# Kernel optimization log

Hardware: AMD Instinct MI355X
Metric: run time of the kernel (lower is better)

The kernel has to match this reference:

```python
import jax, jax.numpy as jnp
import numpy as np

N_NODES = 50000
N_EDGES = 800000
D_IN = 64
D_OUT = 64
EPS = 0.0  # DGL GINConv default init_eps=0, not learnable


def setup_inputs() -> dict:
    key = jax.random.key(0)
    k1, k2, k3, k4, k5 = jax.random.split(key, 5)
    node_inputs = jax.random.normal(k1, (N_NODES, D_IN), dtype=jnp.float32)
    src = jax.random.randint(k2, (N_EDGES,), 0, N_NODES, dtype=jnp.int64)
    dst = jax.random.randint(k3, (N_EDGES,), 0, N_NODES, dtype=jnp.int64)
    # nn.Linear(in_feats, out_feats) params (PyTorch layout: W [out, in])
    bound = 1.0 / np.sqrt(D_IN)
    W = jax.random.uniform(k4, (D_OUT, D_IN), dtype=jnp.float32, minval=-bound, maxval=bound)
    b = jax.random.uniform(k5, (D_OUT,), dtype=jnp.float32, minval=-bound, maxval=bound)
    return {"node_inputs": node_inputs, "W": W, "b": b, "src": src, "dst": dst}


def reference(node_inputs, W, b, src, dst):
    # GIN sum aggregation: for each node, sum features of in-neighbors
    # messages: [E, D_IN] gathered, scatter-summed into [N, D_IN]
    agg = jax.ops.segment_sum(node_inputs[src], dst, num_segments=N_NODES)
    h = (1.0 + EPS) * node_inputs + agg          # [N, D_IN]
    h = h @ W.T + b                              # Linear -> [N, D_OUT]
    h = jnp.tanh(h)
    # Dropout is identity in eval mode (deterministic reference)
    return h
```

## Files before the change

### kernel.cpp

```cpp
#include <hip/hip_runtime.h>
#include <hip/hip_fp16.h>

#define N_NODES 50000
#define N_EDGES 800000
#define D 64

#define NBIN 512
#define BINW 98
#define PBLK 160
#define EPB  5000
#define CAPB 26
#define NCAP 64
#define WGROUP 260

typedef int iv4 __attribute__((ext_vector_type(4)));

__global__ __launch_bounds__(512) void gin_part(const float* __restrict__ x,
                                                const int* __restrict__ src,
                                                const int* __restrict__ dst,
                                                unsigned int* __restrict__ regions,
                                                int* __restrict__ bincnt,
                                                __half* __restrict__ xh) {
    __shared__ int lcnt[NBIN];
    const int tid = threadIdx.x;
    if (tid < NBIN) lcnt[tid] = 0;
    __syncthreads();

    const int ebase = blockIdx.x * EPB;
    unsigned int* __restrict__ rbase = regions + (size_t)blockIdx.x * NBIN * CAPB;

    for (int i = tid; i < EPB / 4; i += 512) {
        const int e = ebase + i * 4;
        const iv4 d4 = *(const iv4*)&dst[e];
        const iv4 s4 = *(const iv4*)&src[e];
        const int dd[4] = {d4.x, d4.y, d4.z, d4.w};
        const int ss[4] = {s4.x, s4.y, s4.z, s4.w};
        #pragma unroll
        for (int j = 0; j < 4; ++j) {
            const int bin = dd[j] / BINW;
            const int pos = atomicAdd(&lcnt[bin], 1);
            if (pos < CAPB)
                rbase[bin * CAPB + pos] = ((unsigned)dd[j] << 16) | (unsigned)ss[j];
        }
    }
    __syncthreads();
    if (tid < NBIN) bincnt[blockIdx.x * NBIN + tid] = lcnt[tid] < CAPB ? lcnt[tid] : CAPB;

    union Pk { uint2 u; __half2 h[2]; };
    uint2* __restrict__ xo = (uint2*)xh;
    for (int i = blockIdx.x * 512 + tid; i < (N_NODES * D) / 4; i += PBLK * 512) {
        const float4 v = *(const float4*)&x[(size_t)i * 4];
        Pk p;
        p.h[0] = __floats2half2_rn(v.x, v.y);
        p.h[1] = __floats2half2_rn(v.z, v.w);
        xo[i] = p.u;
    }
}

__device__ __forceinline__ float fast_tanh(float v) {
    return 1.0f - 2.0f / (__expf(2.0f * v) + 1.0f);
}

__global__ __launch_bounds__(1024, 8) void gin_node(const float* __restrict__ x,
                                                 const __half* __restrict__ xh,
                                                 const float* __restrict__ W,
                                                 const float* __restrict__ bias,
                                                 const unsigned int* __restrict__ regions,
                                                 const int* __restrict__ bincnt,
                                                 float* __restrict__ out) {
    __shared__ alignas(16) unsigned short sbuck[BINW * NCAP];
    __shared__ int   lcnt[BINW];
    __shared__ float Wt2[16 * WGROUP];
    __shared__ float hs[16][4][68];

    const int tid  = threadIdx.x;
    const int lane = tid & 63;
    const int wv   = tid >> 6;
    const int sub  = lane >> 4;
    const int q    = lane & 15;
    const int b    = blockIdx.x;
    const int lo   = b * BINW;

    if (tid < BINW) lcnt[tid] = 0;
    #pragma unroll
    for (int i = tid; i < D * D; i += 1024) {
        const int f = i >> 6, k = i & 63;
        Wt2[(k >> 2) * WGROUP + (f << 2) + (k & 3)] = W[i];
    }
    __syncthreads();

    const int g2 = lane >> 5;
    const int l2 = lane & 31;
    for (int p2 = wv; p2 < PBLK / 2; p2 += 16) {
        const int pb = p2 * 2 + g2;
        const int n = bincnt[pb * NBIN + b];
        if (l2 < n) {
            const unsigned e = regions[((size_t)pb * NBIN + b) * CAPB + l2];
            const int dl  = (int)(e >> 16) - lo;
            const int pos = atomicAdd(&lcnt[dl], 1);
            if (pos < NCAP) sbuck[dl * NCAP + pos] = (unsigned short)(e & 0xffffu);
        }
    }
    __syncthreads();

    const uint2* __restrict__ xr = (const uint2*)xh;
    const float bf = bias[lane];
    const int ncnt   = (wv < 2) ? 7 : 6;
    const int nstart = wv * 6 + ((wv < 2) ? wv : 2);
    const int nend   = nstart + ncnt;

    union Pk { uint2 u; __half2 h[2]; };

    for (int base = nstart; base < nend; base += 4) {
        const int li    = base + sub;
        const bool nv   = (li < nend);
        const int  liC  = nv ? li : (nend - 1);
        const int  node = lo + liC;
        const bool ndv  = nv && (node < N_NODES);
        const int  nodeC = (node < N_NODES) ? node : (N_NODES - 1);

        float4 acc = *(const float4*)&x[(size_t)nodeC * D + (q << 2)];

        int cn = ndv ? lcnt[liC] : 0;
        if (cn > NCAP) cn = NCAP;
        const uint4* __restrict__ slv = (const uint4*)&sbuck[liC * NCAP];

        for (int i = 0; i < cn; i += 8) {
            const int rem = cn - i;
            const uint4 iw = slv[i >> 3];
            int s0 = (int)(iw.x & 0xffffu), s1 = (int)(iw.x >> 16);
            int s2 = (int)(iw.y & 0xffffu), s3 = (int)(iw.y >> 16);
            int s4 = (int)(iw.z & 0xffffu), s5 = (int)(iw.z >> 16);
            int s6 = (int)(iw.w & 0xffffu), s7 = (int)(iw.w >> 16);
            s1 = (1 < rem) ? s1 : 0;  s2 = (2 < rem) ? s2 : 0;
            s3 = (3 < rem) ? s3 : 0;  s4 = (4 < rem) ? s4 : 0;
            s5 = (5 < rem) ? s5 : 0;  s6 = (6 < rem) ? s6 : 0;
            s7 = (7 < rem) ? s7 : 0;
            Pk u0, u1, u2, u3, u4, u5, u6, u7;
            u0.u = xr[(size_t)s0 * 16 + q];  u1.u = xr[(size_t)s1 * 16 + q];
            u2.u = xr[(size_t)s2 * 16 + q];  u3.u = xr[(size_t)s3 * 16 + q];
            u4.u = xr[(size_t)s4 * 16 + q];  u5.u = xr[(size_t)s5 * 16 + q];
            u6.u = xr[(size_t)s6 * 16 + q];  u7.u = xr[(size_t)s7 * 16 + q];
            const float m1 = (1 < rem) ? 1.f : 0.f;
            const float m2 = (2 < rem) ? 1.f : 0.f;
            const float m3 = (3 < rem) ? 1.f : 0.f;
            const float m4 = (4 < rem) ? 1.f : 0.f;
            const float m5 = (5 < rem) ? 1.f : 0.f;
            const float m6 = (6 < rem) ? 1.f : 0.f;
            const float m7 = (7 < rem) ? 1.f : 0.f;
            {
                const float2 a = __half22float2(u0.h[0]), c = __half22float2(u0.h[1]);
                acc.x += a.x; acc.y += a.y; acc.z += c.x; acc.w += c.y;
            }
            {
                const float2 a = __half22float2(u1.h[0]), c = __half22float2(u1.h[1]);
                acc.x = fmaf(a.x, m1, acc.x); acc.y = fmaf(a.y, m1, acc.y);
                acc.z = fmaf(c.x, m1, acc.z); acc.w = fmaf(c.y, m1, acc.w);
            }
            {
                const float2 a = __half22float2(u2.h[0]), c = __half22float2(u2.h[1]);
                acc.x = fmaf(a.x, m2, acc.x); acc.y = fmaf(a.y, m2, acc.y);
                acc.z = fmaf(c.x, m2, acc.z); acc.w = fmaf(c.y, m2, acc.w);
            }
            {
                const float2 a = __half22float2(u3.h[0]), c = __half22float2(u3.h[1]);
                acc.x = fmaf(a.x, m3, acc.x); acc.y = fmaf(a.y, m3, acc.y);
                acc.z = fmaf(c.x, m3, acc.z); acc.w = fmaf(c.y, m3, acc.w);
            }
            {
                const float2 a = __half22float2(u4.h[0]), c = __half22float2(u4.h[1]);
                acc.x = fmaf(a.x, m4, acc.x); acc.y = fmaf(a.y, m4, acc.y);
                acc.z = fmaf(c.x, m4, acc.z); acc.w = fmaf(c.y, m4, acc.w);
            }
            {
                const float2 a = __half22float2(u5.h[0]), c = __half22float2(u5.h[1]);
                acc.x = fmaf(a.x, m5, acc.x); acc.y = fmaf(a.y, m5, acc.y);
                acc.z = fmaf(c.x, m5, acc.z); acc.w = fmaf(c.y, m5, acc.w);
            }
            {
                const float2 a = __half22float2(u6.h[0]), c = __half22float2(u6.h[1]);
                acc.x = fmaf(a.x, m6, acc.x); acc.y = fmaf(a.y, m6, acc.y);
                acc.z = fmaf(c.x, m6, acc.z); acc.w = fmaf(c.y, m6, acc.w);
            }
            {
                const float2 a = __half22float2(u7.h[0]), c = __half22float2(u7.h[1]);
                acc.x = fmaf(a.x, m7, acc.x); acc.y = fmaf(a.y, m7, acc.y);
                acc.z = fmaf(c.x, m7, acc.z); acc.w = fmaf(c.y, m7, acc.w);
            }
        }
        *(float4*)&hs[wv][sub][q << 2] = acc;

        const int left = nend - base;
        const int mcnt = left < 4 ? left : 4;
        const int n0 = lo + base;
        {
            float4 rA = {bf, 0.f, 0.f, 0.f}, rB = rA;
            #pragma unroll 4
            for (int kg = 0; kg < 16; ++kg) {
                const float4 w  = *(const float4*)&Wt2[kg * WGROUP + (lane << 2)];
                const float4 hA = *(const float4*)&hs[wv][0][kg << 2];
                const float4 hB = *(const float4*)&hs[wv][1][kg << 2];
                rA.x = fmaf(hA.x, w.x, rA.x); rA.y = fmaf(hA.y, w.y, rA.y);
                rA.z = fmaf(hA.z, w.z, rA.z); rA.w = fmaf(hA.w, w.w, rA.w);
                rB.x = fmaf(hB.x, w.x, rB.x); rB.y = fmaf(hB.y, w.y, rB.y);
                rB.z = fmaf(hB.z, w.z, rB.z); rB.w = fmaf(hB.w, w.w, rB.w);
            }
            if (n0 < N_NODES)
                out[(size_t)n0 * D + lane] = fast_tanh((rA.x + rA.y) + (rA.z + rA.w));
            if (1 < mcnt && n0 + 1 < N_NODES)
                out[(size_t)(n0 + 1) * D + lane] = fast_tanh((rB.x + rB.y) + (rB.z + rB.w));
        }
        if (2 < mcnt) {
            float4 rC = {bf, 0.f, 0.f, 0.f}, rD = rC;
            #pragma unroll 4
            for (int kg = 0; kg < 16; ++kg) {
                const float4 w  = *(const float4*)&Wt2[kg * WGROUP + (lane << 2)];
                const float4 hC = *(const float4*)&hs[wv][2][kg << 2];
                const float4 hD = *(const float4*)&hs[wv][3][kg << 2];
                rC.x = fmaf(hC.x, w.x, rC.x); rC.y = fmaf(hC.y, w.y, rC.y);
                rC.z = fmaf(hC.z, w.z, rC.z); rC.w = fmaf(hC.w, w.w, rC.w);
                rD.x = fmaf(hD.x, w.x, rD.x); rD.y = fmaf(hD.y, w.y, rD.y);
                rD.z = fmaf(hD.z, w.z, rD.z); rD.w = fmaf(hD.w, w.w, rD.w);
            }
            if (n0 + 2 < N_NODES)
                out[(size_t)(n0 + 2) * D + lane] = fast_tanh((rC.x + rC.y) + (rC.z + rC.w));
            if (3 < mcnt && n0 + 3 < N_NODES)
                out[(size_t)(n0 + 3) * D + lane] = fast_tanh((rD.x + rD.y) + (rD.z + rD.w));
        }
    }
}

extern "C" void kernel_launch(void* const* d_in, const int* in_sizes, int n_in,
                              void* d_out, int out_size, void* d_ws, size_t ws_size,
                              hipStream_t stream) {
    const float* x    = (const float*)d_in[0];
    const float* W    = (const float*)d_in[1];
    const float* bias = (const float*)d_in[2];
    const int*   src  = (const int*)d_in[3];
    const int*   dst  = (const int*)d_in[4];
    float*       out  = (float*)d_out;

    unsigned int* regions = (unsigned int*)d_ws;
    int*          bincnt  = (int*)(regions + (size_t)PBLK * NBIN * CAPB);
    __half*       xh      = (__half*)(bincnt + PBLK * NBIN);

    gin_part<<<PBLK, 512, 0, stream>>>(x, src, dst, regions, bincnt, xh);
    gin_node<<<NBIN, 1024, 0, stream>>>(x, xh, W, bias, regions, bincnt, out);
}
```

Measured before the change: 109.4 us.

## Gather all wave nodes in one pass with 8 lanes per node and 16-byte loads

Each wavefront now gathers neighbor features for all 6-7 of its nodes at once, using 8 lanes per node and 16-byte fp16 loads, instead of two passes of 4 nodes with 16 lanes each. The transform stage is unrolled into fixed pairs of node rows plus an optional seventh. This aims to remove the second gather pass and its serialized latency, and to cut the number of load instructions. In exchange each lane holds more accumulators and the inner loop is only 4 deep, giving fewer loads in flight per iteration and higher register pressure.

After: 112.0 us. 1.02x slower.

```diff
diff --git a/kernel.cpp b/kernel.cpp
--- a/kernel.cpp
+++ b/kernel.cpp
@@ -71,13 +71,13 @@
     __shared__ alignas(16) unsigned short sbuck[BINW * NCAP];
     __shared__ int   lcnt[BINW];
     __shared__ float Wt2[16 * WGROUP];
-    __shared__ float hs[16][4][68];
+    __shared__ float hs[16][8][68];
 
     const int tid  = threadIdx.x;
     const int lane = tid & 63;
     const int wv   = tid >> 6;
-    const int sub  = lane >> 4;
-    const int q    = lane & 15;
+    const int sub8 = lane >> 3;
+    const int q8   = lane & 7;
     const int b    = blockIdx.x;
     const int lo   = b * BINW;
 
@@ -103,130 +103,140 @@
     }
     __syncthreads();
 
-    const uint2* __restrict__ xr = (const uint2*)xh;
+    const uint4* __restrict__ xq = (const uint4*)xh;
     const float bf = bias[lane];
     const int ncnt   = (wv < 2) ? 7 : 6;
     const int nstart = wv * 6 + ((wv < 2) ? wv : 2);
     const int nend   = nstart + ncnt;
 
-    union Pk { uint2 u; __half2 h[2]; };
-
-    for (int base = nstart; base < nend; base += 4) {
-        const int li    = base + sub;
+    union Pk4 { uint4 u; __half2 h[4]; };
+
+    {
+        const int li    = nstart + sub8;
         const bool nv   = (li < nend);
         const int  liC  = nv ? li : (nend - 1);
         const int  node = lo + liC;
         const bool ndv  = nv && (node < N_NODES);
         const int  nodeC = (node < N_NODES) ? node : (N_NODES - 1);
 
-        float4 acc = *(const float4*)&x[(size_t)nodeC * D + (q << 2)];
+        float4 accA = *(const float4*)&x[(size_t)nodeC * D + (q8 << 3)];
+        float4 accB = *(const float4*)&x[(size_t)nodeC * D + (q8 << 3) + 4];
 
         int cn = ndv ? lcnt[liC] : 0;
         if (cn > NCAP) cn = NCAP;
-        const uint4* __restrict__ slv = (const uint4*)&sbuck[liC * NCAP];
-
-        for (int i = 0; i < cn; i += 8) {
+        const uint2* __restrict__ sl2 = (const uint2*)&sbuck[liC * NCAP];
+
+        for (int i = 0; i < cn; i += 4) {
             const int rem = cn - i;
-            const uint4 iw = slv[i >> 3];
+            const uint2 iw = sl2[i >> 2];
             int s0 = (int)(iw.x & 0xffffu), s1 = (int)(iw.x >> 16);
             int s2 = (int)(iw.y & 0xffffu), s3 = (int)(iw.y >> 16);
-            int s4 = (int)(iw.z & 0xffffu), s5 = (int)(iw.z >> 16);
-            int s6 = (int)(iw.w & 0xffffu), s7 = (int)(iw.w >> 16);
             s1 = (1 < rem) ? s1 : 0;  s2 = (2 < rem) ? s2 : 0;
-            s3 = (3 < rem) ? s3 : 0;  s4 = (4 < rem) ? s4 : 0;
-            s5 = (5 < rem) ? s5 : 0;  s6 = (6 < rem) ? s6 : 0;
-            s7 = (7 < rem) ? s7 : 0;
-            Pk u0, u1, u2, u3, u4, u5, u6, u7;
-            u0.u = xr[(size_t)s0 * 16 + q];  u1.u = xr[(size_t)s1 * 16 + q];
-            u2.u = xr[(size_t)s2 * 16 + q];  u3.u = xr[(size_t)s3 * 16 + q];
-            u4.u = xr[(size_t)s4 * 16 + q];  u5.u = xr[(size_t)s5 * 16 + q];
-            u6.u = xr[(size_t)s6 * 16 + q];  u7.u = xr[(size_t)s7 * 16 + q];
+            s3 = (3 < rem) ? s3 : 0;
+            Pk4 u0, u1, u2, u3;
+            u0.u = xq[(size_t)s0 * 8 + q8];  u1.u = xq[(size_t)s1 * 8 + q8];
+            u2.u = xq[(size_t)s2 * 8 + q8];  u3.u = xq[(size_t)s3 * 8 + q8];
             const float m1 = (1 < rem) ? 1.f : 0.f;
             const float m2 = (2 < rem) ? 1.f : 0.f;
             const float m3 = (3 < rem) ? 1.f : 0.f;
-            const float m4 = (4 < rem) ? 1.f : 0.f;
-            const float m5 = (5 < rem) ? 1.f : 0.f;
-            const float m6 = (6 < rem) ? 1.f : 0.f;
-            const float m7 = (7 < rem) ? 1.f : 0.f;
             {
                 const float2 a = __half22float2(u0.h[0]), c = __half22float2(u0.h[1]);
-                acc.x += a.x; acc.y += a.y; acc.z += c.x; acc.w += c.y;
+                const float2 e = __half22float2(u0.h[2]), g = __half22float2(u0.h[3]);
+                accA.x += a.x; accA.y += a.y; accA.z += c.x; accA.w += c.y;
+                accB.x += e.x; accB.y += e.y; accB.z += g.x; accB.w += g.y;
             }
             {
                 const float2 a = __half22float2(u1.h[0]), c = __half22float2(u1.h[1]);
-                acc.x = fmaf(a.x, m1, acc.x); acc.y = fmaf(a.y, m1, acc.y);
-                acc.z = fmaf(c.x, m1, acc.z); acc.w = fmaf(c.y, m1, acc.w);
+                const float2 e = __half22float2(u1.h[2]), g = __half22float2(u1.h[3]);
+                accA.x = fmaf(a.x, m1, accA.x); accA.y = fmaf(a.y, m1, accA.y);
+                accA.z = fmaf(c.x, m1, accA.z); accA.w = fmaf(c.y, m1, accA.w);
+                accB.x = fmaf(e.x, m1, accB.x); accB.y = fmaf(e.y, m1, accB.y);
+                accB.z = fmaf(g.x, m1, accB.z); accB.w = fmaf(g.y, m1, accB.w);
             }
             {
                 const float2 a = __half22float2(u2.h[0]), c = __half22float2(u2.h[1]);
-                acc.x = fmaf(a.x, m2, acc.x); acc.y = fmaf(a.y, m2, acc.y);
-                acc.z = fmaf(c.x, m2, acc.z); acc.w = fmaf(c.y, m2, acc.w);
+                const float2 e = __half22float2(u2.h[2]), g = __half22float2(u2.h[3]);
+                accA.x = fmaf(a.x, m2, accA.x); accA.y = fmaf(a.y, m2, accA.y);
+                accA.z = fmaf(c.x, m2, accA.z); accA.w = fmaf(c.y, m2, accA.w);
+                accB.x = fmaf(e.x, m2, accB.x); accB.y = fmaf(e.y, m2, accB.y);
+                accB.z = fmaf(g.x, m2, accB.z); accB.w = fmaf(g.y, m2, accB.w);
             }
             {
                 const float2 a = __half22float2(u3.h[0]), c = __half22float2(u3.h[1]);
-                acc.x = fmaf(a.x, m3, acc.x); acc.y = fmaf(a.y, m3, acc.y);
-                acc.z = fmaf(c.x, m3, acc.z); acc.w = fmaf(c.y, m3, acc.w);
-            }
-            {
-                const float2 a = __half22float2(u4.h[0]), c = __half22float2(u4.h[1]);
-                acc.x = fmaf(a.x, m4, acc.x); acc.y = fmaf(a.y, m4, acc.y);
-                acc.z = fmaf(c.x, m4, acc.z); acc.w = fmaf(c.y, m4, acc.w);
-            }
-            {
-                const float2 a = __half22float2(u5.h[0]), c = __half22float2(u5.h[1]);
-                acc.x = fmaf(a.x, m5, acc.x); acc.y = fmaf(a.y, m5, acc.y);
-                acc.z = fmaf(c.x, m5, acc.z); acc.w = fmaf(c.y, m5, acc.w);
-            }
-            {
-                const float2 a = __half22float2(u6.h[0]), c = __half22float2(u6.h[1]);
-                acc.x = fmaf(a.x, m6, acc.x); acc.y = fmaf(a.y, m6, acc.y);
-                acc.z = fmaf(c.x, m6, acc.z); acc.w = fmaf(c.y, m6, acc.w);
-            }
-            {
-                const float2 a = __half22float2(u7.h[0]), c = __half22float2(u7.h[1]);
-                acc.x = fmaf(a.x, m7, acc.x); acc.y = fmaf(a.y, m7, acc.y);
-                acc.z = fmaf(c.x, m7, acc.z); acc.w = fmaf(c.y, m7, acc.w);
-            }
-        }
-        *(float4*)&hs[wv][sub][q << 2] = acc;
-
-        const int left = nend - base;
-        const int mcnt = left < 4 ? left : 4;
-        const int n0 = lo + base;
-        {
-            float4 rA = {bf, 0.f, 0.f, 0.f}, rB = rA;
-            #pragma unroll 4
-            for (int kg = 0; kg < 16; ++kg) {
-                const float4 w  = *(const float4*)&Wt2[kg * WGROUP + (lane << 2)];
-                const float4 hA = *(const float4*)&hs[wv][0][kg << 2];
-                const float4 hB = *(const float4*)&hs[wv][1][kg << 2];
-                rA.x = fmaf(hA.x, w.x, rA.x); rA.y = fmaf(hA.y, w.y, rA.y);
-                rA.z = fmaf(hA.z, w.z, rA.z); rA.w = fmaf(hA.w, w.w, rA.w);
-                rB.x = fmaf(hB.x, w.x, rB.x); rB.y = fmaf(hB.y, w.y, rB.y);
-                rB.z = fmaf(hB.z, w.z, rB.z); rB.w = fmaf(hB.w, w.w, rB.w);
-            }
-            if (n0 < N_NODES)
-                out[(size_t)n0 * D + lane] = fast_tanh((rA.x + rA.y) + (rA.z + rA.w));
-            if (1 < mcnt && n0 + 1 < N_NODES)
-                out[(size_t)(n0 + 1) * D + lane] = fast_tanh((rB.x + rB.y) + (rB.z + rB.w));
-        }
-        if (2 < mcnt) {
-            float4 rC = {bf, 0.f, 0.f, 0.f}, rD = rC;
-            #pragma unroll 4
-            for (int kg = 0; kg < 16; ++kg) {
-                const float4 w  = *(const float4*)&Wt2[kg * WGROUP + (lane << 2)];
-                const float4 hC = *(const float4*)&hs[wv][2][kg << 2];
-                const float4 hD = *(const float4*)&hs[wv][3][kg << 2];
-                rC.x = fmaf(hC.x, w.x, rC.x); rC.y = fmaf(hC.y, w.y, rC.y);
-                rC.z = fmaf(hC.z, w.z, rC.z); rC.w = fmaf(hC.w, w.w, rC.w);
-                rD.x = fmaf(hD.x, w.x, rD.x); rD.y = fmaf(hD.y, w.y, rD.y);
-                rD.z = fmaf(hD.z, w.z, rD.z); rD.w = fmaf(hD.w, w.w, rD.w);
-            }
-            if (n0 + 2 < N_NODES)
-                out[(size_t)(n0 + 2) * D + lane] = fast_tanh((rC.x + rC.y) + (rC.z + rC.w));
-            if (3 < mcnt && n0 + 3 < N_NODES)
-                out[(size_t)(n0 + 3) * D + lane] = fast_tanh((rD.x + rD.y) + (rD.z + rD.w));
-        }
+                const float2 e = __half22float2(u3.h[2]), g = __half22float2(u3.h[3]);
+                accA.x = fmaf(a.x, m3, accA.x); accA.y = fmaf(a.y, m3, accA.y);
+                accA.z = fmaf(c.x, m3, accA.z); accA.w = fmaf(c.y, m3, accA.w);
+                accB.x = fmaf(e.x, m3, accB.x); accB.y = fmaf(e.y, m3, accB.y);
+                accB.z = fmaf(g.x, m3, accB.z); accB.w = fmaf(g.y, m3, accB.w);
+            }
+        }
+        *(float4*)&hs[wv][sub8][q8 << 3]       = accA;
+        *(float4*)&hs[wv][sub8][(q8 << 3) + 4] = accB;
+    }
+
+    const int n0 = lo + nstart;
+    {
+        float4 rA = {bf, 0.f, 0.f, 0.f}, rB = rA;
+        #pragma unroll 4
+        for (int kg = 0; kg < 16; ++kg) {
+            const float4 w  = *(const float4*)&Wt2[kg * WGROUP + (lane << 2)];
+            const float4 hA = *(const float4*)&hs[wv][0][kg << 2];
+            const float4 hB = *(const float4*)&hs[wv][1][kg << 2];
+            rA.x = fmaf(hA.x, w.x, rA.x); rA.y = fmaf(hA.y, w.y, rA.y);
+            rA.z = fmaf(hA.z, w.z, rA.z); rA.w = fmaf(hA.w, w.w, rA.w);
+            rB.x = fmaf(hB.x, w.x, rB.x); rB.y = fmaf(hB.y, w.y, rB.y);
+            rB.z = fmaf(hB.z, w.z, rB.z); rB.w = fmaf(hB.w, w.w, rB.w);
+        }
+        if (n0 < N_NODES)
+            out[(size_t)n0 * D + lane] = fast_tanh((rA.x + rA.y) + (rA.z + rA.w));
+        if (n0 + 1 < N_NODES)
+            out[(size_t)(n0 + 1) * D + lane] = fast_tanh((rB.x + rB.y) + (rB.z + rB.w));
+    }
+    {
+        float4 rC = {bf, 0.f, 0.f, 0.f}, rD = rC;
+        #pragma unroll 4
+        for (int kg = 0; kg < 16; ++kg) {
+            const float4 w  = *(const float4*)&Wt2[kg * WGROUP + (lane << 2)];
+            const float4 hC = *(const float4*)&hs[wv][2][kg << 2];
+            const float4 hD = *(const float4*)&hs[wv][3][kg << 2];
+            rC.x = fmaf(hC.x, w.x, rC.x); rC.y = fmaf(hC.y, w.y, rC.y);
+            rC.z = fmaf(hC.z, w.z, rC.z); rC.w = fmaf(hC.w, w.w, rC.w);
+            rD.x = fmaf(hD.x, w.x, rD.x); rD.y = fmaf(hD.y, w.y, rD.y);
+            rD.z = fmaf(hD.z, w.z, rD.z); rD.w = fmaf(hD.w, w.w, rD.w);
+        }
+        if (n0 + 2 < N_NODES)
+            out[(size_t)(n0 + 2) * D + lane] = fast_tanh((rC.x + rC.y) + (rC.z + rC.w));
+        if (n0 + 3 < N_NODES)
+            out[(size_t)(n0 + 3) * D + lane] = fast_tanh((rD.x + rD.y) + (rD.z + rD.w));
+    }
+    {
+        float4 rE = {bf, 0.f, 0.f, 0.f}, rF = rE;
+        #pragma unroll 4
+        for (int kg = 0; kg < 16; ++kg) {
+            const float4 w  = *(const float4*)&Wt2[kg * WGROUP + (lane << 2)];
+            const float4 hE = *(const float4*)&hs[wv][4][kg << 2];
+            const float4 hF = *(const float4*)&hs[wv][5][kg << 2];
+            rE.x = fmaf(hE.x, w.x, rE.x); rE.y = fmaf(hE.y, w.y, rE.y);
+            rE.z = fmaf(hE.z, w.z, rE.z); rE.w = fmaf(hE.w, w.w, rE.w);
+            rF.x = fmaf(hF.x, w.x, rF.x); rF.y = fmaf(hF.y, w.y, rF.y);
+            rF.z = fmaf(hF.z, w.z, rF.z); rF.w = fmaf(hF.w, w.w, rF.w);
+        }
+        if (n0 + 4 < N_NODES)
+            out[(size_t)(n0 + 4) * D + lane] = fast_tanh((rE.x + rE.y) + (rE.z + rE.w));
+        if (n0 + 5 < N_NODES)
+            out[(size_t)(n0 + 5) * D + lane] = fast_tanh((rF.x + rF.y) + (rF.z + rF.w));
+    }
+    if (ncnt == 7) {
+        float4 rG = {bf, 0.f, 0.f, 0.f};
+        #pragma unroll 4
+        for (int kg = 0; kg < 16; ++kg) {
+            const float4 w  = *(const float4*)&Wt2[kg * WGROUP + (lane << 2)];
+            const float4 hG = *(const float4*)&hs[wv][6][kg << 2];
+            rG.x = fmaf(hG.x, w.x, rG.x); rG.y = fmaf(hG.y, w.y, rG.y);
+            rG.z = fmaf(hG.z, w.z, rG.z); rG.w = fmaf(hG.w, w.w, rG.w);
+        }
+        if (n0 + 6 < N_NODES)
+            out[(size_t)(n0 + 6) * D + lane] = fast_tanh((rG.x + rG.y) + (rG.z + rG.w));
     }
 }
 
```
